# Optimization experiments

Hardware: AMD Instinct MI355X
Metric: run time of the kernel (lower is better)

## Reference

```python
import jax, jax.numpy as jnp
import numpy as np

D = 128      # internal_dimensions
L = 4        # num_edge_convs
N = 100000   # nodes
E = 800000   # edges
G = 64       # graphs
IN = 4       # in_channels


def _ln(x, g, b):
    m = jnp.mean(x, -1, keepdims=True)
    v = jnp.mean((x - m) ** 2, -1, keepdims=True)
    return (x - m) * jax.lax.rsqrt(v + 1e-5) * g + b


def _gelu(x):
    return jax.nn.gelu(x, approximate=False)  # torch nn.GELU default (erf)


def _seg_mean(x, seg, n):
    s = jax.ops.segment_sum(x, seg, num_segments=n)
    c = jax.ops.segment_sum(jnp.ones((x.shape[0], 1), x.dtype), seg, num_segments=n)
    return s / jnp.maximum(c, 1.0)


def _seg_max(x, seg, n):
    m = jax.ops.segment_max(x, seg, num_segments=n)
    return jnp.where(jnp.isfinite(m), m, 0.0)  # empty segments -> 0 (PyG convention)


def _forward(x, edge_index, batch, num_graphs,
             in_W1, in_b1, in_g1, in_bn1, in_W2, in_b2, in_g2, in_bn2,
             pre_g, pre_b, cW1, cb1, cg1, cbb1, cW2, cb2, cg2, cbb2, pW, pb,
             ag_g, ag_b,
             kW1, kb1, kg1, kbb1, kW2, kb2, kg2, kbb2,
             kW3, kb3, kg3, kbb3, kW4, kb4):
    n = x.shape[0]
    # input_net: Linear -> LN -> GELU -> Linear -> LN   (dropout=0, eval)
    h = _gelu(_ln(x @ in_W1 + in_b1, in_g1, in_bn1))
    h = _ln(h @ in_W2 + in_b2, in_g2, in_bn2)

    x_in_max = _seg_max(h, batch, num_graphs)
    x_in_mean = _seg_mean(h, batch, num_graphs)

    src, dst = edge_index[0], edge_index[1]  # PyG: message from src (x_j) to dst (x_i)
    xcur = h
    for l in range(L):
        identity = xcur
        hn = _ln(xcur, pre_g[l], pre_b[l])
        xi = hn[dst]            # [E, D]
        xj = hn[src]            # [E, D]
        m = jnp.concatenate([xi, xj - xi], axis=-1)       # [E, 2D]
        m = _gelu(_ln(m @ cW1[l] + cb1[l], cg1[l], cbb1[l]))
        m = _gelu(_ln(m @ cW2[l] + cb2[l], cg2[l], cbb2[l]))
        a_max = _seg_max(m, dst, n)
        a_mean = _seg_mean(m, dst, n)
        aggr = jnp.concatenate([a_max, a_mean], axis=-1)  # [N, 2D]
        xcur = identity + aggr @ pW[l] + pb[l]

    xcur = _ln(xcur, ag_g, ag_b)
    x_g_max = _seg_max(xcur, batch, num_graphs)
    x_g_mean = _seg_mean(xcur, batch, num_graphs)

    xp = jnp.concatenate([x_in_max, x_in_mean, x_g_max, x_g_mean], axis=-1)  # [G, 4D]
    z = _gelu(_ln(xp @ kW1 + kb1, kg1, kbb1))
    z = _gelu(_ln(z @ kW2 + kb2, kg2, kbb2))
    z = _gelu(_ln(z @ kW3 + kb3, kg3, kbb3))
    return z @ kW4 + kb4  # [G, 1]


def setup_inputs() -> dict:
    key = jax.random.key(0)
    ks = iter(jax.random.split(key, 64))
    def W(shape, fan):
        return jax.random.normal(next(ks), shape, jnp.float32) * np.float32((2.0 / fan) ** 0.5)
    inp = {}
    inp["x"] = jax.random.normal(next(ks), (N, IN), jnp.float32)
    inp["edge_index"] = jax.random.randint(next(ks), (2, E), 0, N)
    inp["batch"] = jnp.sort(jax.random.randint(next(ks), (N,), 0, G))
    inp["num_graphs"] = G
    inp["in_W1"] = W((IN, D), IN); inp["in_b1"] = jnp.zeros((D,), jnp.float32)
    inp["in_g1"] = jnp.ones((D,), jnp.float32); inp["in_bn1"] = jnp.zeros((D,), jnp.float32)
    inp["in_W2"] = W((D, D), D); inp["in_b2"] = jnp.zeros((D,), jnp.float32)
    inp["in_g2"] = jnp.ones((D,), jnp.float32); inp["in_bn2"] = jnp.zeros((D,), jnp.float32)
    inp["pre_g"] = jnp.ones((L, D), jnp.float32); inp["pre_b"] = jnp.zeros((L, D), jnp.float32)
    inp["cW1"] = W((L, 2 * D, D), 2 * D); inp["cb1"] = jnp.zeros((L, D), jnp.float32)
    inp["cg1"] = jnp.ones((L, D), jnp.float32); inp["cbb1"] = jnp.zeros((L, D), jnp.float32)
    inp["cW2"] = W((L, D, D), D); inp["cb2"] = jnp.zeros((L, D), jnp.float32)
    inp["cg2"] = jnp.ones((L, D), jnp.float32); inp["cbb2"] = jnp.zeros((L, D), jnp.float32)
    inp["pW"] = W((L, 2 * D, D), 2 * D); inp["pb"] = jnp.zeros((L, D), jnp.float32)
    inp["ag_g"] = jnp.ones((D,), jnp.float32); inp["ag_b"] = jnp.zeros((D,), jnp.float32)
    inp["kW1"] = W((4 * D, D), 4 * D); inp["kb1"] = jnp.zeros((D,), jnp.float32)
    inp["kg1"] = jnp.ones((D,), jnp.float32); inp["kbb1"] = jnp.zeros((D,), jnp.float32)
    inp["kW2"] = W((D, D), D); inp["kb2"] = jnp.zeros((D,), jnp.float32)
    inp["kg2"] = jnp.ones((D,), jnp.float32); inp["kbb2"] = jnp.zeros((D,), jnp.float32)
    inp["kW3"] = W((D, D // 4), D); inp["kb3"] = jnp.zeros((D // 4,), jnp.float32)
    inp["kg3"] = jnp.ones((D // 4,), jnp.float32); inp["kbb3"] = jnp.zeros((D // 4,), jnp.float32)
    inp["kW4"] = W((D // 4, 1), D // 4); inp["kb4"] = jnp.zeros((1,), jnp.float32)
    return inp


def reference(x, edge_index, batch, num_graphs,
              in_W1, in_b1, in_g1, in_bn1, in_W2, in_b2, in_g2, in_bn2,
              pre_g, pre_b, cW1, cb1, cg1, cbb1, cW2, cb2, cg2, cbb2, pW, pb,
              ag_g, ag_b,
              kW1, kb1, kg1, kbb1, kW2, kb2, kg2, kbb2,
              kW3, kb3, kg3, kbb3, kW4, kb4):
    return _forward(x, edge_index, batch, num_graphs,
                    in_W1, in_b1, in_g1, in_bn1, in_W2, in_b2, in_g2, in_bn2,
                    pre_g, pre_b, cW1, cb1, cg1, cbb1, cW2, cb2, cg2, cbb2, pW, pb,
                    ag_g, ag_b,
                    kW1, kb1, kg1, kbb1, kW2, kb2, kg2, kbb2,
                    kW3, kb3, kg3, kbb3, kW4, kb4)
```

## Files before the change

kernel.cpp:

```cpp
#include <hip/hip_runtime.h>
#include <hip/hip_bf16.h>
#include <math.h>

__device__ __forceinline__ float geluf(float x) {
    return 0.5f * x * (1.0f + erff(x * 0.70710678118654752f));
}
#define MAPNEGINF 0x007FFFFFu
__device__ __forceinline__ float funmap(unsigned m) {
    return __uint_as_float((m & 0x80000000u) ? (m ^ 0x80000000u) : ~m);
}
__device__ __forceinline__ unsigned fmap(float f) {
    unsigned u = __float_as_uint(f);
    return ((int)u < 0) ? ~u : (u | 0x80000000u);
}
__device__ __forceinline__ float wred64(float v) {
#pragma unroll
    for (int m = 1; m < 64; m <<= 1) v += __shfl_xor(v, m);
    return v;
}
__device__ __forceinline__ unsigned short bf16r(float f) {
    unsigned u = __float_as_uint(f);
    u += 0x7fffu + ((u >> 16) & 1u);
    return (unsigned short)(u >> 16);
}

__device__ __forceinline__ void stage_wq(float* Ws, const float* __restrict__ src, int t) {
#pragma unroll
    for (int it = 0; it < 4; ++it) {
        const int idx = it * 1024 + (t << 2);
        *(float4*)(Ws + idx) = *(const float4*)(src + idx);
    }
}

__device__ __forceinline__ void kloop_q(const float* As, const float* Ws, float (&acc)[4][8],
                                        const int r0, const int ogc, const int kb) {
#pragma unroll
    for (int kk = 0; kk < 32; kk += 4) {
        const float4 a0 = *(const float4*)(As + (r0 + 0) * 132 + kb + kk);
        const float4 a1 = *(const float4*)(As + (r0 + 1) * 132 + kb + kk);
        const float4 a2 = *(const float4*)(As + (r0 + 2) * 132 + kb + kk);
        const float4 a3 = *(const float4*)(As + (r0 + 3) * 132 + kb + kk);
#define MAD8(R, AV)                                                                     \
    {                                                                                   \
        acc[R][0] += (AV)*wA.x; acc[R][1] += (AV)*wA.y; acc[R][2] += (AV)*wA.z;         \
        acc[R][3] += (AV)*wA.w; acc[R][4] += (AV)*wB.x; acc[R][5] += (AV)*wB.y;         \
        acc[R][6] += (AV)*wB.z; acc[R][7] += (AV)*wB.w;                                 \
    }
#define KSTEP(J, C)                                                                     \
    {                                                                                   \
        const float4 wA = *(const float4*)(Ws + (kk + (J)) * 128 + ogc);                \
        const float4 wB = *(const float4*)(Ws + (kk + (J)) * 128 + 64 + ogc);           \
        MAD8(0, a0.C) MAD8(1, a1.C) MAD8(2, a2.C) MAD8(3, a3.C)                         \
    }
        KSTEP(0, x) KSTEP(1, y) KSTEP(2, z) KSTEP(3, w)
#undef KSTEP
#undef MAD8
    }
}

__global__ void k_zero(unsigned* __restrict__ p, int n) {
    const int i = blockIdx.x * 256 + threadIdx.x;
    if (i < n) p[i] = 0u;
}

__global__ void k_copyu(const unsigned* __restrict__ a, const unsigned* __restrict__ b,
                        unsigned* __restrict__ ac, unsigned* __restrict__ bc, int n) {
    const int i = blockIdx.x * 256 + threadIdx.x;
    if (i < n) {
        ac[i] = a[i];
        bc[i] = b[i];
    }
}

__global__ void k_count(const int* __restrict__ ei, unsigned* __restrict__ deg, int E) {
    const int e = blockIdx.x * 256 + threadIdx.x;
    if (e < E) atomicAdd(deg + ei[E + e], 1u);
}

__global__ void k_scan1(const unsigned* __restrict__ deg, unsigned* __restrict__ excl,
                        unsigned* __restrict__ bsum, int n) {
    __shared__ unsigned sh[256];
    const int t = threadIdx.x;
    const int base = blockIdx.x * 1024 + t * 4;
    unsigned v0 = (base + 0 < n) ? deg[base + 0] : 0u;
    unsigned v1 = (base + 1 < n) ? deg[base + 1] : 0u;
    unsigned v2 = (base + 2 < n) ? deg[base + 2] : 0u;
    unsigned v3 = (base + 3 < n) ? deg[base + 3] : 0u;
    const unsigned s = v0 + v1 + v2 + v3;
    sh[t] = s;
    __syncthreads();
    for (int off = 1; off < 256; off <<= 1) {
        unsigned x = 0;
        if (t >= off) x = sh[t - off];
        __syncthreads();
        if (t >= off) sh[t] += x;
        __syncthreads();
    }
    const unsigned ebase = sh[t] - s;
    if (base + 0 < n) excl[base + 0] = ebase;
    if (base + 1 < n) excl[base + 1] = ebase + v0;
    if (base + 2 < n) excl[base + 2] = ebase + v0 + v1;
    if (base + 3 < n) excl[base + 3] = ebase + v0 + v1 + v2;
    if (t == 255) bsum[blockIdx.x] = sh[255];
}

__global__ void k_scan2(unsigned* __restrict__ bsum, int nb) {
    __shared__ unsigned sh[256];
    const int t = threadIdx.x;
    const unsigned v = (t < nb) ? bsum[t] : 0u;
    sh[t] = v;
    __syncthreads();
    for (int off = 1; off < 256; off <<= 1) {
        unsigned x = 0;
        if (t >= off) x = sh[t - off];
        __syncthreads();
        if (t >= off) sh[t] += x;
        __syncthreads();
    }
    if (t < nb) bsum[t] = sh[t] - v;
}

__global__ void k_scan3(unsigned* __restrict__ excl, const unsigned* __restrict__ bsum, int n) {
    const int t = threadIdx.x;
    const int base = blockIdx.x * 1024 + t * 4;
    const unsigned add = bsum[blockIdx.x];
#pragma unroll
    for (int j = 0; j < 4; ++j)
        if (base + j < n) excl[base + j] += add;
}

__global__ void k_scatter(const int* __restrict__ ei, unsigned* __restrict__ cursor,
                          int* __restrict__ esrc, int* __restrict__ edst, int E) {
    const int e = blockIdx.x * 256 + threadIdx.x;
    if (e < E) {
        const int s = ei[e];
        const int d = ei[E + e];
        const unsigned pos = atomicAdd(cursor + d, 1u);
        esrc[pos] = s;
        edst[pos] = d;
    }
}

__global__ void k_in(const float* __restrict__ x, const float* __restrict__ W1,
                     const float* __restrict__ b1, const float* __restrict__ g1,
                     const float* __restrict__ bn1, const float* __restrict__ W2,
                     const float* __restrict__ b2, const float* __restrict__ g2,
                     const float* __restrict__ bn2, float* __restrict__ C, int n) {
    __shared__ float As[64 * 132];
    __shared__ float Ws[4096];
    __shared__ float W1s[512];
    const int t = threadIdx.x;
    const int n0 = blockIdx.x * 64;
    if (t < 128) {
        W1s[t] = W1[t];
        W1s[128 + t] = W1[128 + t];
        W1s[256 + t] = W1[256 + t];
        W1s[384 + t] = W1[384 + t];
    }
    __syncthreads();
    {
        const int r = t >> 2, c0 = (t & 3) << 5;
        const int row = n0 + r;
        float4 xv = make_float4(0.f, 0.f, 0.f, 0.f);
        if (row < n) xv = *(const float4*)(x + (size_t)row * 4);
        float hv[32];
        float s = 0.f, q = 0.f;
#pragma unroll
        for (int j = 0; j < 32; ++j) {
            const int c = c0 + j;
            const float z = b1[c] + xv.x * W1s[c] + xv.y * W1s[128 + c] +
                            xv.z * W1s[256 + c] + xv.w * W1s[384 + c];
            hv[j] = z;
            s += z;
            q += z * z;
        }
        s += __shfl_xor(s, 1); s += __shfl_xor(s, 2);
        q += __shfl_xor(q, 1); q += __shfl_xor(q, 2);
        const float mean = s * 0.0078125f;
        const float var = q * 0.0078125f - mean * mean;
        const float rs = rsqrtf(var + 1e-5f);
#pragma unroll
        for (int j = 0; j < 32; ++j) {
            const int c = c0 + j;
            As[r * 132 + c] = geluf((hv[j] - mean) * rs * g1[c] + bn1[c]);
        }
    }
    float acc[4][8];
#pragma unroll
    for (int r = 0; r < 4; ++r)
#pragma unroll
        for (int o = 0; o < 8; ++o) acc[r][o] = 0.f;
    const int og = t & 15, eg = t >> 4;
    const int ogc = og << 2, r0 = eg << 2;
#pragma unroll
    for (int q4 = 0; q4 < 4; ++q4) {
        stage_wq(Ws, W2 + q4 * 4096, t);
        __syncthreads();
        kloop_q(As, Ws, acc, r0, ogc, q4 * 32);
        __syncthreads();
    }
    const float4 bA = *(const float4*)(b2 + ogc);
    const float4 bB = *(const float4*)(b2 + 64 + ogc);
    const float4 gA = *(const float4*)(g2 + ogc);
    const float4 gB = *(const float4*)(g2 + 64 + ogc);
    const float4 lA = *(const float4*)(bn2 + ogc);
    const float4 lB = *(const float4*)(bn2 + 64 + ogc);
#pragma unroll
    for (int r = 0; r < 4; ++r) {
        float v[8];
        v[0] = acc[r][0] + bA.x; v[1] = acc[r][1] + bA.y;
        v[2] = acc[r][2] + bA.z; v[3] = acc[r][3] + bA.w;
        v[4] = acc[r][4] + bB.x; v[5] = acc[r][5] + bB.y;
        v[6] = acc[r][6] + bB.z; v[7] = acc[r][7] + bB.w;
        float s = 0.f, q = 0.f;
#pragma unroll
        for (int o = 0; o < 8; ++o) { s += v[o]; q += v[o] * v[o]; }
#pragma unroll
        for (int m = 1; m < 16; m <<= 1) { s += __shfl_xor(s, m); q += __shfl_xor(q, m); }
        const float mean = s * 0.0078125f;
        const float var = q * 0.0078125f - mean * mean;
        const float rs = rsqrtf(var + 1e-5f);
        const int row = n0 + r0 + r;
        if (row < n) {
            *(float4*)(C + (size_t)row * 128 + ogc) = make_float4(
                (v[0] - mean) * rs * gA.x + lA.x, (v[1] - mean) * rs * gA.y + lA.y,
                (v[2] - mean) * rs * gA.z + lA.z, (v[3] - mean) * rs * gA.w + lA.w);
            *(float4*)(C + (size_t)row * 128 + 64 + ogc) = make_float4(
                (v[4] - mean) * rs * gB.x + lB.x, (v[5] - mean) * rs * gB.y + lB.y,
                (v[6] - mean) * rs * gB.z + lB.z, (v[7] - mean) * rs * gB.w + lB.w);
        }
    }
}

__global__ void k_ln(const float* __restrict__ in, const float* __restrict__ g,
                     const float* __restrict__ b, float* __restrict__ out, int n) {
    const int t = threadIdx.x, lane = t & 63, wave = t >> 6;
    const int d0 = lane << 1;
    const float ga = g[d0], gb = g[d0 + 1], ba = b[d0], bb = b[d0 + 1];
    const int stride = gridDim.x * 4;
    for (int node = blockIdx.x * 4 + wave; node < n; node += stride) {
        const float2 v = *(const float2*)(in + (size_t)node * 128 + d0);
        const float s = wred64(v.x + v.y), q = wred64(v.x * v.x + v.y * v.y);
        const float mean = s * 0.0078125f, var = q * 0.0078125f - mean * mean;
        const float rs = rsqrtf(var + 1e-5f);
        *(float2*)(out + (size_t)node * 128 + d0) =
            make_float2((v.x - mean) * rs * ga + ba, (v.y - mean) * rs * gb + bb);
    }
}

__global__ void k_pq2(const float* __restrict__ xcur, const float* __restrict__ g,
                      const float* __restrict__ b, const float* __restrict__ cW1,
                      const float* __restrict__ cb1, unsigned short* __restrict__ P,
                      unsigned short* __restrict__ Q, int n) {
    __shared__ float As[64 * 132];
    __shared__ float Ws[4096];
    __shared__ float sg[128], sb[128];
    const int t = threadIdx.x;
    const int n0 = blockIdx.x * 64;
    if (t < 128) { sg[t] = g[t]; sb[t] = b[t]; }
    __syncthreads();
    {
        const int r = t >> 2, c0 = (t & 3) << 5;
        const int row = n0 + r;
        const bool ok = row < n;
        float4 v4[8];
        float s = 0.f, q = 0.f;
        if (ok) {
#pragma unroll
            for (int j = 0; j < 8; ++j) {
                v4[j] = *(const float4*)(xcur + (size_t)row * 128 + c0 + (j << 2));
                s += v4[j].x + v4[j].y + v4[j].z + v4[j].w;
                q += v4[j].x * v4[j].x + v4[j].y * v4[j].y + v4[j].z * v4[j].z +
                     v4[j].w * v4[j].w;
            }
        } else {
#pragma unroll
            for (int j = 0; j < 8; ++j) v4[j] = make_float4(0.f, 0.f, 0.f, 0.f);
        }
        s += __shfl_xor(s, 1); s += __shfl_xor(s, 2);
        q += __shfl_xor(q, 1); q += __shfl_xor(q, 2);
        const float mean = s * 0.0078125f;
        const float var = q * 0.0078125f - mean * mean;
        const float rs = rsqrtf(var + 1e-5f);
#pragma unroll
        for (int j = 0; j < 8; ++j) {
            const int c = c0 + (j << 2);
            As[r * 132 + c + 0] = (v4[j].x - mean) * rs * sg[c + 0] + sb[c + 0];
            As[r * 132 + c + 1] = (v4[j].y - mean) * rs * sg[c + 1] + sb[c + 1];
            As[r * 132 + c + 2] = (v4[j].z - mean) * rs * sg[c + 2] + sb[c + 2];
            As[r * 132 + c + 3] = (v4[j].w - mean) * rs * sg[c + 3] + sb[c + 3];
        }
    }
    float accP[4][8], accQ[4][8];
#pragma unroll
    for (int r = 0; r < 4; ++r)
#pragma unroll
        for (int o = 0; o < 8; ++o) { accP[r][o] = 0.f; accQ[r][o] = 0.f; }
    const int og = t & 15, eg = t >> 4;
    const int ogc = og << 2, r0 = eg << 2;
#pragma unroll
    for (int q4 = 0; q4 < 4; ++q4) {
        stage_wq(Ws, cW1 + q4 * 4096, t);
        __syncthreads();
        kloop_q(As, Ws, accP, r0, ogc, q4 * 32);
        __syncthreads();
        stage_wq(Ws, cW1 + 16384 + q4 * 4096, t);
        __syncthreads();
        kloop_q(As, Ws, accQ, r0, ogc, q4 * 32);
        __syncthreads();
    }
    const float4 bA = *(const float4*)(cb1 + ogc);
    const float4 bB = *(const float4*)(cb1 + 64 + ogc);
#pragma unroll
    for (int r = 0; r < 4; ++r) {
        const int row = n0 + r0 + r;
        if (row < n) {
            ushort4 p0, p1, q0, q1;
            p0.x = bf16r(accP[r][0] - accQ[r][0] + bA.x);
            p0.y = bf16r(accP[r][1] - accQ[r][1] + bA.y);
            p0.z = bf16r(accP[r][2] - accQ[r][2] + bA.z);
            p0.w = bf16r(accP[r][3] - accQ[r][3] + bA.w);
            p1.x = bf16r(accP[r][4] - accQ[r][4] + bB.x);
            p1.y = bf16r(accP[r][5] - accQ[r][5] + bB.y);
            p1.z = bf16r(accP[r][6] - accQ[r][6] + bB.z);
            p1.w = bf16r(accP[r][7] - accQ[r][7] + bB.w);
            q0.x = bf16r(accQ[r][0]); q0.y = bf16r(accQ[r][1]);
            q0.z = bf16r(accQ[r][2]); q0.w = bf16r(accQ[r][3]);
            q1.x = bf16r(accQ[r][4]); q1.y = bf16r(accQ[r][5]);
            q1.z = bf16r(accQ[r][6]); q1.w = bf16r(accQ[r][7]);
            *(ushort4*)(P + (size_t)row * 128 + ogc) = p0;
            *(ushort4*)(P + (size_t)row * 128 + 64 + ogc) = p1;
            *(ushort4*)(Q + (size_t)row * 128 + ogc) = q0;
            *(ushort4*)(Q + (size_t)row * 128 + 64 + ogc) = q1;
        }
    }
}

__global__ __launch_bounds__(256, 2) void k_edge(
    const unsigned short* __restrict__ P, const unsigned short* __restrict__ Q,
    const int* __restrict__ esrc, const int* __restrict__ edst, const float* __restrict__ W2,
    const float* __restrict__ g1, const float* __restrict__ b1, const float* __restrict__ cb2,
    const float* __restrict__ g2, const float* __restrict__ b2,
    const unsigned* __restrict__ rowend, const unsigned* __restrict__ degc,
    const float* __restrict__ pW, float* __restrict__ upd, float* __restrict__ recmax,
    float* __restrict__ recsum, int* __restrict__ recid, int E) {
    __shared__ float Us[64 * 132];
    __shared__ float Ws[4096];
    __shared__ int sdst[64], ssrc[64], sdg[64];
    __shared__ float scb2[128], sg2[128], sb2[128];
    __shared__ float smx[128], ssm[128], spart[256];
    const int t = threadIdx.x;
    const int base = blockIdx.x * 512;
    if (t >= 128) {
        const int d = t - 128;
        scb2[d] = cb2[d];
        sg2[d] = g2[d];
        sb2[d] = b2[d];
    }
    const int lane = t & 63, wave = t >> 6;
    const int d0 = lane << 1;
    const float g1a = g1[d0], g1b = g1[d0 + 1], b1a = b1[d0], b1b = b1[d0 + 1];
    const int og = t & 15, eg = t >> 4;
    const int ogc = og << 2, r0 = eg << 2;
    int cur = -1, istart = 0;
    float vmax = -INFINITY, vsum = 0.f;
    int id0 = -1, id1 = -1;

    auto flushrun = [&](int iend) {
        const unsigned re = rowend[cur];
        const unsigned dg = degc[cur];
        const unsigned rs0 = re - dg;
        const unsigned ps = (unsigned)(base + istart), pe = (unsigned)(base + iend);
        if (ps == rs0 && pe == re) {
            if (t < 128) {
                smx[t] = vmax;
                ssm[t] = vsum / (float)dg;
            }
            __syncthreads();
            {
                const int d = t & 127;
                const float* wc = pW + ((t >> 7) ? 16384 : 0) + d;
                const float* sv = (t >> 7) ? ssm : smx;
                float a = 0.f;
#pragma unroll 8
                for (int k = 0; k < 128; ++k) a += sv[k] * wc[(size_t)k << 7];
                spart[t] = a;
            }
            __syncthreads();
            if (t < 128) upd[(size_t)cur * 128 + t] = spart[t] + spart[t + 128];
        } else {
            const int slot = (istart == 0) ? 0 : 1;
            if (t < 128) {
                const size_t ro = (size_t)(2 * blockIdx.x + slot) * 128 + t;
                recmax[ro] = vmax;
                recsum[ro] = vsum;
            }
            if (slot == 0) id0 = cur; else id1 = cur;
        }
    };

    for (int s8 = 0; s8 < 8; ++s8) {
        const int sb = base + s8 * 64;
        __syncthreads();
        if (t < 64) {
            const int idx = sb + t;
            const int ci = idx < E ? idx : (E - 1);
            ssrc[t] = esrc[ci];
            const int d = edst[ci];
            sdg[t] = d;
            sdst[t] = (idx < E) ? d : -1;
        }
        __syncthreads();
#pragma unroll 4
        for (int p = 0; p < 16; ++p) {
            const int i = (p << 2) + wave;
            const unsigned pu = *(const unsigned*)(P + ((size_t)sdg[i] << 7) + d0);
            const unsigned qu = *(const unsigned*)(Q + ((size_t)ssrc[i] << 7) + d0);
            const float x0 = __uint_as_float(pu << 16) + __uint_as_float(qu << 16);
            const float x1 =
                __uint_as_float(pu & 0xffff0000u) + __uint_as_float(qu & 0xffff0000u);
            const float s = wred64(x0 + x1);
            const float q = wred64(x0 * x0 + x1 * x1);
            const float mean = s * 0.0078125f;
            const float var = q * 0.0078125f - mean * mean;
            const float rs = rsqrtf(var + 1e-5f);
            const float y0 = geluf((x0 - mean) * rs * g1a + b1a);
            const float y1 = geluf((x1 - mean) * rs * g1b + b1b);
            *(float2*)(Us + i * 132 + d0) = make_float2(y0, y1);
        }
        float acc[4][8];
#pragma unroll
        for (int r = 0; r < 4; ++r)
#pragma unroll
            for (int o = 0; o < 8; ++o) acc[r][o] = 0.f;
#pragma unroll
        for (int q4 = 0; q4 < 4; ++q4) {
            stage_wq(Ws, W2 + q4 * 4096, t);
            __syncthreads();
            kloop_q(Us, Ws, acc, r0, ogc, q4 * 32);
            __syncthreads();
        }
#pragma unroll
        for (int r = 0; r < 4; ++r) {
            float v[8];
            float s = 0.f, q = 0.f;
#pragma unroll
            for (int o = 0; o < 8; ++o) {
                const int col = (o < 4) ? (ogc + o) : (64 + ogc + o - 4);
                v[o] = acc[r][o] + scb2[col];
                s += v[o];
                q += v[o] * v[o];
            }
#pragma unroll
            for (int m = 1; m < 16; m <<= 1) { s += __shfl_xor(s, m); q += __shfl_xor(q, m); }
            const float mean = s * 0.0078125f;
            const float var = q * 0.0078125f - mean * mean;
            const float rs = rsqrtf(var + 1e-5f);
#pragma unroll
            for (int o = 0; o < 8; ++o) {
                const int col = (o < 4) ? (ogc + o) : (64 + ogc + o - 4);
                v[o] = geluf((v[o] - mean) * rs * sg2[col] + sb2[col]);
            }
            *(float4*)(Us + (r0 + r) * 132 + ogc) = make_float4(v[0], v[1], v[2], v[3]);
            *(float4*)(Us + (r0 + r) * 132 + 64 + ogc) = make_float4(v[4], v[5], v[6], v[7]);
        }
        __syncthreads();
        for (int i = 0; i < 64; ++i) {
            const int dn = sdst[i];
            const int gi = s8 * 64 + i;
            if (dn != cur) {
                if (cur >= 0) flushrun(gi);
                cur = dn;
                istart = gi;
                vmax = -INFINITY;
                vsum = 0.f;
            }
            if (dn >= 0 && t < 128) {
                const float v = Us[i * 132 + t];
                vmax = fmaxf(vmax, v);
                vsum += v;
            }
        }
    }
    if (cur >= 0) flushrun(min(512, E - base));
    if (t == 0) {
        recid[2 * blockIdx.x] = id0;
        recid[2 * blockIdx.x + 1] = id1;
    }
}

__global__ void k_merge2(const unsigned* __restrict__ rowend, const unsigned* __restrict__ degc,
                         const float* __restrict__ recmax, const float* __restrict__ recsum,
                         const int* __restrict__ recid, const float* __restrict__ pW,
                         float* __restrict__ upd, int n) {
    __shared__ float sm[128], ss[128];
    const int node = blockIdx.x;
    const int d = threadIdx.x;
    if (node >= n) return;
    const unsigned dg = degc[node];
    if (dg == 0u) {
        upd[(size_t)node * 128 + d] = 0.f;
        return;
    }
    const unsigned re = rowend[node], rs = re - dg;
    const int b0 = rs >> 9, b1 = (re - 1) >> 9;
    if (b0 == b1) return;
    float m = -INFINITY, s = 0.f;
    for (int b = b0; b <= b1; ++b) {
#pragma unroll
        for (int sl = 0; sl < 2; ++sl) {
            if (recid[2 * b + sl] == node) {
                const size_t ro = (size_t)(2 * b + sl) * 128 + d;
                m = fmaxf(m, recmax[ro]);
                s += recsum[ro];
            }
        }
    }
    sm[d] = m;
    ss[d] = s / (float)dg;
    __syncthreads();
    float a = 0.f;
#pragma unroll 8
    for (int k = 0; k < 128; ++k)
        a += sm[k] * pW[(size_t)k * 128 + d] + ss[k] * pW[(size_t)(128 + k) * 128 + d];
    upd[(size_t)node * 128 + d] = a;
}

__global__ void k_updS(const float* __restrict__ upd, const float* __restrict__ pb,
                       float* __restrict__ xcur, int n32) {
    for (int i = blockIdx.x * 256 + threadIdx.x; i < n32; i += gridDim.x * 256) {
        const int c4 = (i & 31) << 2;
        const float4 u = ((const float4*)upd)[i];
        const float4 pv = *(const float4*)(pb + c4);
        const float4 xv = ((const float4*)xcur)[i];
        ((float4*)xcur)[i] =
            make_float4(xv.x + u.x + pv.x, xv.y + u.y + pv.y, xv.z + u.z + pv.z,
                        xv.w + u.w + pv.w);
    }
}

__global__ void k_pool_init(unsigned* __restrict__ gmax1, float* __restrict__ gsum1,
                            unsigned* __restrict__ gcount1, unsigned* __restrict__ gmax2,
                            float* __restrict__ gsum2, unsigned* __restrict__ gcount2, int ng) {
    const int i = blockIdx.x * 256 + threadIdx.x;
    if (i < ng * 128) {
        gmax1[i] = MAPNEGINF;
        gsum1[i] = 0.f;
        gmax2[i] = MAPNEGINF;
        gsum2[i] = 0.f;
    }
    if (i < ng) {
        gcount1[i] = 0u;
        gcount2[i] = 0u;
    }
}

__global__ void k_pool(const float* __restrict__ in, const int* __restrict__ batch,
                       unsigned* __restrict__ gmax, float* __restrict__ gsum,
                       unsigned* __restrict__ gcount, int n) {
    const int t = threadIdx.x;
    if (t >= 128) return;
    const int per = (n + gridDim.x - 1) / gridDim.x;
    const int i0 = blockIdx.x * per;
    const int i1 = min(n, i0 + per);
    if (i0 >= i1) return;
    int cur = batch[i0];
    float vmax = -INFINITY, vsum = 0.f;
    unsigned cnt = 0;
    for (int i = i0; i < i1; ++i) {
        const int g = batch[i];
        if (g != cur) {
            atomicMax(gmax + (size_t)cur * 128 + t, fmap(vmax));
            atomicAdd(gsum + (size_t)cur * 128 + t, vsum);
            if (t == 0) atomicAdd(gcount + cur, cnt);
            cur = g;
            vmax = -INFINITY;
            vsum = 0.f;
            cnt = 0;
        }
        const float v = in[(size_t)i * 128 + t];
        vmax = fmaxf(vmax, v);
        vsum += v;
        cnt++;
    }
    atomicMax(gmax + (size_t)cur * 128 + t, fmap(vmax));
    atomicAdd(gsum + (size_t)cur * 128 + t, vsum);
    if (t == 0) atomicAdd(gcount + cur, cnt);
}

__global__ void k_xp(const unsigned* __restrict__ gmax1, const float* __restrict__ gsum1,
                     const unsigned* __restrict__ gcount1, const unsigned* __restrict__ gmax2,
                     const float* __restrict__ gsum2, const unsigned* __restrict__ gcount2,
                     float* __restrict__ xp) {
    const int g = blockIdx.x, d = threadIdx.x;
    const unsigned c1u = gcount1[g], c2u = gcount2[g];
    const float c1 = (float)(c1u < 1u ? 1u : c1u);
    const float c2 = (float)(c2u < 1u ? 1u : c2u);
    const unsigned m1 = gmax1[g * 128 + d], m2 = gmax2[g * 128 + d];
    xp[g * 512 + d] = (m1 == MAPNEGINF) ? 0.f : funmap(m1);
    xp[g * 512 + 128 + d] = gsum1[g * 128 + d] / c1;
    xp[g * 512 + 256 + d] = (m2 == MAPNEGINF) ? 0.f : funmap(m2);
    xp[g * 512 + 384 + d] = gsum2[g * 128 + d] / c2;
}

__global__ __launch_bounds__(64) void k_know(
    const float* __restrict__ xp, const float* __restrict__ kW1, const float* __restrict__ kb1,
    const float* __restrict__ kg1, const float* __restrict__ kbb1, const float* __restrict__ kW2,
    const float* __restrict__ kb2, const float* __restrict__ kg2, const float* __restrict__ kbb2,
    const float* __restrict__ kW3, const float* __restrict__ kb3, const float* __restrict__ kg3,
    const float* __restrict__ kbb3, const float* __restrict__ kW4, const float* __restrict__ kb4,
    float* __restrict__ out) {
    __shared__ float sh[512];
    __shared__ float s3[32];
    const int l = threadIdx.x, g = blockIdx.x;
    const int d0 = l << 1;
    *(float4*)(sh + l * 8) = *(const float4*)(xp + g * 512 + l * 8);
    *(float4*)(sh + l * 8 + 4) = *(const float4*)(xp + g * 512 + l * 8 + 4);
    __syncthreads();
    float a0 = kb1[d0], a1 = kb1[d0 + 1];
    for (int k = 0; k < 512; ++k) {
        const float u = sh[k];
        const float2 w = *(const float2*)(kW1 + k * 128 + d0);
        a0 += u * w.x;
        a1 += u * w.y;
    }
    {
        const float s = wred64(a0 + a1), q = wred64(a0 * a0 + a1 * a1);
        const float mean = s * 0.0078125f, var = q * 0.0078125f - mean * mean;
        const float rs = rsqrtf(var + 1e-5f);
        a0 = geluf((a0 - mean) * rs * kg1[d0] + kbb1[d0]);
        a1 = geluf((a1 - mean) * rs * kg1[d0 + 1] + kbb1[d0 + 1]);
    }
    __syncthreads();
    sh[d0] = a0;
    sh[d0 + 1] = a1;
    __syncthreads();
    float b0v = kb2[d0], b1v = kb2[d0 + 1];
    for (int k = 0; k < 128; ++k) {
        const float u = sh[k];
        const float2 w = *(const float2*)(kW2 + k * 128 + d0);
        b0v += u * w.x;
        b1v += u * w.y;
    }
    {
        const float s = wred64(b0v + b1v), q = wred64(b0v * b0v + b1v * b1v);
        const float mean = s * 0.0078125f, var = q * 0.0078125f - mean * mean;
        const float rs = rsqrtf(var + 1e-5f);
        b0v = geluf((b0v - mean) * rs * kg2[d0] + kbb2[d0]);
        b1v = geluf((b1v - mean) * rs * kg2[d0 + 1] + kbb2[d0 + 1]);
    }
    __syncthreads();
    sh[d0] = b0v;
    sh[d0 + 1] = b1v;
    __syncthreads();
    const int d3 = (l & 15) << 1;
    float c0 = kb3[d3], c1 = kb3[d3 + 1];
    for (int k = 0; k < 128; ++k) {
        const float u = sh[k];
        const float2 w = *(const float2*)(kW3 + k * 32 + d3);
        c0 += u * w.x;
        c1 += u * w.y;
    }
    {
        float s = c0 + c1, q = c0 * c0 + c1 * c1;
#pragma unroll
        for (int m = 1; m < 16; m <<= 1) {
            s += __shfl_xor(s, m);
            q += __shfl_xor(q, m);
        }
        const float mean = s * 0.03125f, var = q * 0.03125f - mean * mean;
        const float rs = rsqrtf(var + 1e-5f);
        c0 = geluf((c0 - mean) * rs * kg3[d3] + kbb3[d3]);
        c1 = geluf((c1 - mean) * rs * kg3[d3 + 1] + kbb3[d3 + 1]);
    }
    if (l < 16) {
        s3[d3] = c0;
        s3[d3 + 1] = c1;
    }
    __syncthreads();
    if (l == 0) {
        float rr = kb4[0];
        for (int k = 0; k < 32; ++k) rr += s3[k] * kW4[k];
        out[g] = rr;
    }
}

extern "C" void kernel_launch(void* const* d_in, const int* in_sizes, int n_in, void* d_out,
                              int out_size, void* d_ws, size_t ws_size, hipStream_t stream) {
    const int N = in_sizes[0] / 4;
    const int E = in_sizes[1] / 2;
    const int G = 64;
    const int L = 4;

    const float* x = (const float*)d_in[0];
    const int* ei = (const int*)d_in[1];
    const int* batch = (const int*)d_in[2];
    const float* inW1 = (const float*)d_in[4];
    const float* inb1 = (const float*)d_in[5];
    const float* ing1 = (const float*)d_in[6];
    const float* inbn1 = (const float*)d_in[7];
    const float* inW2 = (const float*)d_in[8];
    const float* inb2 = (const float*)d_in[9];
    const float* ing2 = (const float*)d_in[10];
    const float* inbn2 = (const float*)d_in[11];
    const float* pre_g = (const float*)d_in[12];
    const float* pre_b = (const float*)d_in[13];
    const float* cW1 = (const float*)d_in[14];
    const float* cb1 = (const float*)d_in[15];
    const float* cg1 = (const float*)d_in[16];
    const float* cbb1 = (const float*)d_in[17];
    const float* cW2 = (const float*)d_in[18];
    const float* cb2 = (const float*)d_in[19];
    const float* cg2 = (const float*)d_in[20];
    const float* cbb2 = (const float*)d_in[21];
    const float* pW = (const float*)d_in[22];
    const float* pb = (const float*)d_in[23];
    const float* ag_g = (const float*)d_in[24];
    const float* ag_b = (const float*)d_in[25];
    const float* kW1 = (const float*)d_in[26];
    const float* kb1 = (const float*)d_in[27];
    const float* kg1 = (const float*)d_in[28];
    const float* kbb1 = (const float*)d_in[29];
    const float* kW2 = (const float*)d_in[30];
    const float* kb2 = (const float*)d_in[31];
    const float* kg2 = (const float*)d_in[32];
    const float* kbb2 = (const float*)d_in[33];
    const float* kW3 = (const float*)d_in[34];
    const float* kb3 = (const float*)d_in[35];
    const float* kg3 = (const float*)d_in[36];
    const float* kbb3 = (const float*)d_in[37];
    const float* kW4 = (const float*)d_in[38];
    const float* kb4 = (const float*)d_in[39];
    float* out = (float*)d_out;

    const int nblkE = (E + 511) / 512;

    char* wsb = (char*)d_ws;
    size_t off = 0;
    auto ALC = [&](size_t bytes) {
        void* p = wsb + off;
        off = (off + bytes + 255) & ~(size_t)255;
        return p;
    };
    const size_t NB = (size_t)N * 128 * 4;
    float* xcur = (float*)ALC(NB);
    float* upd = (float*)ALC(NB);
    unsigned short* Pb = (unsigned short*)ALC((size_t)N * 128 * 2);
    unsigned short* Qb = (unsigned short*)ALC((size_t)N * 128 * 2);
    unsigned* deg = (unsigned*)ALC((size_t)N * 4);
    unsigned* cursor = (unsigned*)ALC((size_t)N * 4);
    unsigned* degc = (unsigned*)ALC((size_t)N * 4);
    unsigned* rowend = (unsigned*)ALC((size_t)N * 4);
    unsigned* bsum = (unsigned*)ALC(4096);
    int* esrc = (int*)ALC((size_t)E * 4);
    int* edst = (int*)ALC((size_t)E * 4);
    float* recmax = (float*)ALC((size_t)nblkE * 2 * 128 * 4);
    float* recsum = (float*)ALC((size_t)nblkE * 2 * 128 * 4);
    int* recid = (int*)ALC((size_t)nblkE * 2 * 4);
    unsigned* gmax1 = (unsigned*)ALC((size_t)G * 128 * 4);
    float* gsum1 = (float*)ALC((size_t)G * 128 * 4);
    unsigned* gcount1 = (unsigned*)ALC((size_t)G * 4);
    unsigned* gmax2 = (unsigned*)ALC((size_t)G * 128 * 4);
    float* gsum2 = (float*)ALC((size_t)G * 128 * 4);
    unsigned* gcount2 = (unsigned*)ALC((size_t)G * 4);
    float* xp = (float*)ALC((size_t)G * 512 * 4);

    if (off > ws_size) {
        k_zero<<<(out_size + 255) / 256, 256, 0, stream>>>((unsigned*)d_out, out_size);
        return;
    }

    k_zero<<<(N + 255) / 256, 256, 0, stream>>>(deg, N);
    k_count<<<(E + 255) / 256, 256, 0, stream>>>(ei, deg, E);
    const int nb = (N + 1023) / 1024;
    k_scan1<<<nb, 256, 0, stream>>>(deg, cursor, bsum, N);
    k_scan2<<<1, 256, 0, stream>>>(bsum, nb);
    k_scan3<<<nb, 256, 0, stream>>>(cursor, bsum, N);
    k_scatter<<<(E + 255) / 256, 256, 0, stream>>>(ei, cursor, esrc, edst, E);
    k_copyu<<<(N + 255) / 256, 256, 0, stream>>>(deg, cursor, degc, rowend, N);

    const int grid64 = (N + 63) / 64;
    k_in<<<grid64, 256, 0, stream>>>(x, inW1, inb1, ing1, inbn1, inW2, inb2, ing2, inbn2, xcur,
                                     N);
    k_pool_init<<<(G * 128 + 255) / 256, 256, 0, stream>>>(gmax1, gsum1, gcount1, gmax2, gsum2,
                                                           gcount2, G);
    k_pool<<<512, 256, 0, stream>>>(xcur, batch, gmax1, gsum1, gcount1, N);

    for (int l = 0; l < L; ++l) {
        k_pq2<<<grid64, 256, 0, stream>>>(xcur, pre_g + l * 128, pre_b + l * 128,
                                          cW1 + (size_t)l * 32768, cb1 + l * 128, Pb, Qb, N);
        k_edge<<<nblkE, 256, 0, stream>>>(Pb, Qb, esrc, edst, cW2 + (size_t)l * 16384,
                                          cg1 + l * 128, cbb1 + l * 128, cb2 + l * 128,
                                          cg2 + l * 128, cbb2 + l * 128, rowend, degc,
                                          pW + (size_t)l * 32768, upd, recmax, recsum, recid, E);
        k_merge2<<<N, 128, 0, stream>>>(rowend, degc, recmax, recsum, recid,
                                        pW + (size_t)l * 32768, upd, N);
        k_updS<<<2048, 256, 0, stream>>>(upd, pb + l * 128, xcur, N * 32);
    }

    k_ln<<<1024, 256, 0, stream>>>(xcur, ag_g, ag_b, upd, N);
    k_pool<<<512, 256, 0, stream>>>(upd, batch, gmax2, gsum2, gcount2, N);
    k_xp<<<G, 128, 0, stream>>>(gmax1, gsum1, gcount1, gmax2, gsum2, gcount2, xp);
    k_know<<<G, 64, 0, stream>>>(xp, kW1, kb1, kg1, kbb1, kW2, kb2, kg2, kbb2, kW3, kb3, kg3,
                                 kbb3, kW4, kb4, out);
}
```

Measured before the change: 82.25 ms.

## Fuse residual update into pq/lnpool kernels and dedupe destination gathers in edge kernel

Removes the separate residual-update kernel by folding xcur+upd+pb into the next layer's LN/projection kernel, and fuses the final LayerNorm with graph pooling into a single pass. In the edge kernel, each 64-edge chunk is segmented by destination with a wave prefix scan, so each distinct P row is gathered once into shared memory and reused by the other edges in its run. This cuts global traffic and kernel launches, at the cost of extra shared memory (16KB) and barriers in the edge kernel, which may lower occupancy.

```diff
diff --git a/kernel.cpp b/kernel.cpp
--- a/kernel.cpp
+++ b/kernel.cpp
@@ -232,26 +232,11 @@
     }
 }
 
-__global__ void k_ln(const float* __restrict__ in, const float* __restrict__ g,
-                     const float* __restrict__ b, float* __restrict__ out, int n) {
-    const int t = threadIdx.x, lane = t & 63, wave = t >> 6;
-    const int d0 = lane << 1;
-    const float ga = g[d0], gb = g[d0 + 1], ba = b[d0], bb = b[d0 + 1];
-    const int stride = gridDim.x * 4;
-    for (int node = blockIdx.x * 4 + wave; node < n; node += stride) {
-        const float2 v = *(const float2*)(in + (size_t)node * 128 + d0);
-        const float s = wred64(v.x + v.y), q = wred64(v.x * v.x + v.y * v.y);
-        const float mean = s * 0.0078125f, var = q * 0.0078125f - mean * mean;
-        const float rs = rsqrtf(var + 1e-5f);
-        *(float2*)(out + (size_t)node * 128 + d0) =
-            make_float2((v.x - mean) * rs * ga + ba, (v.y - mean) * rs * gb + bb);
-    }
-}
-
-__global__ void k_pq2(const float* __restrict__ xcur, const float* __restrict__ g,
-                      const float* __restrict__ b, const float* __restrict__ cW1,
-                      const float* __restrict__ cb1, unsigned short* __restrict__ P,
-                      unsigned short* __restrict__ Q, int n) {
+__global__ void k_pq(float* __restrict__ xcur, const float* __restrict__ upd,
+                     const float* __restrict__ pbl, const float* __restrict__ g,
+                     const float* __restrict__ b, const float* __restrict__ cW1,
+                     const float* __restrict__ cb1, unsigned short* __restrict__ P,
+                     unsigned short* __restrict__ Q, int n) {
     __shared__ float As[64 * 132];
     __shared__ float Ws[4096];
     __shared__ float sg[128], sb[128];
@@ -268,10 +253,18 @@
         if (ok) {
 #pragma unroll
             for (int j = 0; j < 8; ++j) {
-                v4[j] = *(const float4*)(xcur + (size_t)row * 128 + c0 + (j << 2));
-                s += v4[j].x + v4[j].y + v4[j].z + v4[j].w;
-                q += v4[j].x * v4[j].x + v4[j].y * v4[j].y + v4[j].z * v4[j].z +
-                     v4[j].w * v4[j].w;
+                const int c = c0 + (j << 2);
+                float4 xv = *(const float4*)(xcur + (size_t)row * 128 + c);
+                if (upd) {
+                    const float4 u = *(const float4*)(upd + (size_t)row * 128 + c);
+                    const float4 pv = *(const float4*)(pbl + c);
+                    xv = make_float4(xv.x + u.x + pv.x, xv.y + u.y + pv.y, xv.z + u.z + pv.z,
+                                     xv.w + u.w + pv.w);
+                    *(float4*)(xcur + (size_t)row * 128 + c) = xv;
+                }
+                v4[j] = xv;
+                s += xv.x + xv.y + xv.z + xv.w;
+                q += xv.x * xv.x + xv.y * xv.y + xv.z * xv.z + xv.w * xv.w;
             }
         } else {
 #pragma unroll
@@ -346,7 +339,9 @@
     float* __restrict__ recsum, int* __restrict__ recid, int E) {
     __shared__ float Us[64 * 132];
     __shared__ float Ws[4096];
+    __shared__ unsigned Pcu[64 * 64];
     __shared__ int sdst[64], ssrc[64], sdg[64];
+    __shared__ unsigned char srid[64], sfirst[64];
     __shared__ float scb2[128], sg2[128], sb2[128];
     __shared__ float smx[128], ssm[128], spart[256];
     const int t = threadIdx.x;
@@ -411,11 +406,34 @@
             sdst[t] = (idx < E) ? d : -1;
         }
         __syncthreads();
+        if (t < 64) {
+            const int first = (t == 0) ? 1 : (sdg[t] != sdg[t - 1]);
+            int scanv = first;
+#pragma unroll
+            for (int o = 1; o < 64; o <<= 1) {
+                const int up = __shfl_up(scanv, o);
+                if (lane >= o) scanv += up;
+            }
+            sfirst[t] = (unsigned char)first;
+            srid[t] = (unsigned char)(scanv - 1);
+        }
+        __syncthreads();
+        unsigned quv[16];
 #pragma unroll 4
         for (int p = 0; p < 16; ++p) {
             const int i = (p << 2) + wave;
-            const unsigned pu = *(const unsigned*)(P + ((size_t)sdg[i] << 7) + d0);
-            const unsigned qu = *(const unsigned*)(Q + ((size_t)ssrc[i] << 7) + d0);
+            quv[p] = *(const unsigned*)(Q + ((size_t)ssrc[i] << 7) + d0);
+            if (sfirst[i]) {
+                Pcu[(int)srid[i] * 64 + lane] =
+                    *(const unsigned*)(P + ((size_t)sdg[i] << 7) + d0);
+            }
+        }
+        __syncthreads();
+#pragma unroll 4
+        for (int p = 0; p < 16; ++p) {
+            const int i = (p << 2) + wave;
+            const unsigned pu = Pcu[(int)srid[i] * 64 + lane];
+            const unsigned qu = quv[p];
             const float x0 = __uint_as_float(pu << 16) + __uint_as_float(qu << 16);
             const float x1 =
                 __uint_as_float(pu & 0xffff0000u) + __uint_as_float(qu & 0xffff0000u);
@@ -526,16 +544,86 @@
     upd[(size_t)node * 128 + d] = a;
 }
 
-__global__ void k_updS(const float* __restrict__ upd, const float* __restrict__ pb,
-                       float* __restrict__ xcur, int n32) {
-    for (int i = blockIdx.x * 256 + threadIdx.x; i < n32; i += gridDim.x * 256) {
-        const int c4 = (i & 31) << 2;
-        const float4 u = ((const float4*)upd)[i];
-        const float4 pv = *(const float4*)(pb + c4);
-        const float4 xv = ((const float4*)xcur)[i];
-        ((float4*)xcur)[i] =
-            make_float4(xv.x + u.x + pv.x, xv.y + u.y + pv.y, xv.z + u.z + pv.z,
-                        xv.w + u.w + pv.w);
+__global__ void k_lnpool(const float* __restrict__ xcur, const float* __restrict__ upd,
+                         const float* __restrict__ pbl, const float* __restrict__ g,
+                         const float* __restrict__ b, const int* __restrict__ batch,
+                         unsigned* __restrict__ gmax, float* __restrict__ gsum,
+                         unsigned* __restrict__ gcount, int n) {
+    __shared__ float Ys[64 * 132];
+    __shared__ int sbt[64];
+    const int t = threadIdx.x;
+    const int n0 = blockIdx.x * 64;
+    if (t < 64) {
+        const int node = n0 + t;
+        sbt[t] = (node < n) ? batch[node] : -1;
+    }
+    {
+        const int r = t >> 2, c0 = (t & 3) << 5;
+        const int row = n0 + r;
+        const bool ok = row < n;
+        float4 v4[8];
+        float s = 0.f, q = 0.f;
+        if (ok) {
+#pragma unroll
+            for (int j = 0; j < 8; ++j) {
+                const int c = c0 + (j << 2);
+                const float4 xv = *(const float4*)(xcur + (size_t)row * 128 + c);
+                const float4 u = *(const float4*)(upd + (size_t)row * 128 + c);
+                const float4 pv = *(const float4*)(pbl + c);
+                v4[j] = make_float4(xv.x + u.x + pv.x, xv.y + u.y + pv.y, xv.z + u.z + pv.z,
+                                    xv.w + u.w + pv.w);
+                s += v4[j].x + v4[j].y + v4[j].z + v4[j].w;
+                q += v4[j].x * v4[j].x + v4[j].y * v4[j].y + v4[j].z * v4[j].z +
+                     v4[j].w * v4[j].w;
+            }
+        } else {
+#pragma unroll
+            for (int j = 0; j < 8; ++j) v4[j] = make_float4(0.f, 0.f, 0.f, 0.f);
+        }
+        s += __shfl_xor(s, 1); s += __shfl_xor(s, 2);
+        q += __shfl_xor(q, 1); q += __shfl_xor(q, 2);
+        const float mean = s * 0.0078125f;
+        const float var = q * 0.0078125f - mean * mean;
+        const float rs = rsqrtf(var + 1e-5f);
+#pragma unroll
+        for (int j = 0; j < 8; ++j) {
+            const int c = c0 + (j << 2);
+            Ys[r * 132 + c + 0] = (v4[j].x - mean) * rs * g[c + 0] + b[c + 0];
+            Ys[r * 132 + c + 1] = (v4[j].y - mean) * rs * g[c + 1] + b[c + 1];
+            Ys[r * 132 + c + 2] = (v4[j].z - mean) * rs * g[c + 2] + b[c + 2];
+            Ys[r * 132 + c + 3] = (v4[j].w - mean) * rs * g[c + 3] + b[c + 3];
+        }
+    }
+    __syncthreads();
+    if (t < 128) {
+        int curg = -1;
+        float vmax = -INFINITY, vsum = 0.f;
+        unsigned cnt = 0;
+        for (int i = 0; i < 64; ++i) {
+            const int gid = sbt[i];
+            if (gid != curg) {
+                if (curg >= 0) {
+                    atomicMax(gmax + (size_t)curg * 128 + t, fmap(vmax));
+                    atomicAdd(gsum + (size_t)curg * 128 + t, vsum);
+                    if (t == 0) atomicAdd(gcount + curg, cnt);
+                }
+                curg = gid;
+                vmax = -INFINITY;
+                vsum = 0.f;
+                cnt = 0;
+            }
+            if (gid >= 0) {
+                const float v = Ys[i * 132 + t];
+                vmax = fmaxf(vmax, v);
+                vsum += v;
+                cnt++;
+            }
+        }
+        if (curg >= 0) {
+            atomicMax(gmax + (size_t)curg * 128 + t, fmap(vmax));
+            atomicAdd(gsum + (size_t)curg * 128 + t, vsum);
+            if (t == 0) atomicAdd(gcount + curg, cnt);
+        }
     }
 }
 
@@ -787,19 +875,20 @@
     k_pool<<<512, 256, 0, stream>>>(xcur, batch, gmax1, gsum1, gcount1, N);
 
     for (int l = 0; l < L; ++l) {
-        k_pq2<<<grid64, 256, 0, stream>>>(xcur, pre_g + l * 128, pre_b + l * 128,
-                                          cW1 + (size_t)l * 32768, cb1 + l * 128, Pb, Qb, N);
+        k_pq<<<grid64, 256, 0, stream>>>(xcur, (l == 0) ? (const float*)nullptr : upd,
+                                         (l == 0) ? (const float*)nullptr : (pb + (l - 1) * 128),
+                                         pre_g + l * 128, pre_b + l * 128,
+                                         cW1 + (size_t)l * 32768, cb1 + l * 128, Pb, Qb, N);
         k_edge<<<nblkE, 256, 0, stream>>>(Pb, Qb, esrc, edst, cW2 + (size_t)l * 16384,
                                           cg1 + l * 128, cbb1 + l * 128, cb2 + l * 128,
                                           cg2 + l * 128, cbb2 + l * 128, rowend, degc,
                                           pW + (size_t)l * 32768, upd, recmax, recsum, recid, E);
         k_merge2<<<N, 128, 0, stream>>>(rowend, degc, recmax, recsum, recid,
                                         pW + (size_t)l * 32768, upd, N);
-        k_updS<<<2048, 256, 0, stream>>>(upd, pb + l * 128, xcur, N * 32);
-    }
-
-    k_ln<<<1024, 256, 0, stream>>>(xcur, ag_g, ag_b, upd, N);
-    k_pool<<<512, 256, 0, stream>>>(upd, batch, gmax2, gsum2, gcount2, N);
+    }
+
+    k_lnpool<<<grid64, 256, 0, stream>>>(xcur, upd, pb + 3 * 128, ag_g, ag_b, batch, gmax2,
+                                         gsum2, gcount2, N);
     k_xp<<<G, 128, 0, stream>>>(gmax1, gsum1, gcount1, gmax2, gsum2, gcount2, xp);
     k_know<<<G, 64, 0, stream>>>(xp, kW1, kb1, kg1, kbb1, kW2, kb2, kg2, kbb2, kW3, kb3, kg3,
                                  kbb3, kW4, kb4, out);
```

Result: no change. 83.73 ms (+1.8%).
